# Optimization experiments

Measured on AMD Instinct MI355X. Metric: run time of the kernel, lower is better.

## Reference

```python
import jax, jax.numpy as jnp
import numpy as np

EPS = 1e-5

def _mvn(feat):
    # instance-norm style mean/std over spatial dims; torch .var is unbiased (ddof=1)
    b, c = feat.shape[:2]
    flat = feat.reshape(b, c, -1)
    mu = flat.mean(-1)[:, :, None, None]
    std = jnp.sqrt(flat.var(-1, ddof=1) + EPS)[:, :, None, None]
    return (feat - mu) / std

def setup_inputs() -> dict:
    key = jax.random.key(0)
    ks = jax.random.split(key, 10)
    B, C, H, W = 4, 512, 64, 64
    sc = 0.05
    return {
        "content": jax.random.normal(ks[0], (B, C, H, W), jnp.float32),
        "style": jax.random.normal(ks[1], (B, C, H, W), jnp.float32),
        "content_key": jax.random.normal(ks[2], (B, C, H, W), jnp.float32),
        "style_key": jax.random.normal(ks[3], (B, C, H, W), jnp.float32),
        "Wf": jax.random.normal(ks[4], (C, C), jnp.float32) * sc,
        "bf": jax.random.normal(ks[5], (C,), jnp.float32) * sc,
        "Wg": jax.random.normal(ks[6], (C, C), jnp.float32) * sc,
        "bg": jax.random.normal(ks[7], (C,), jnp.float32) * sc,
        "Wh": jax.random.normal(ks[8], (C, C), jnp.float32) * sc,
        "bh": jax.random.normal(ks[9], (C,), jnp.float32) * sc,
    }

def reference(content, style, content_key, style_key, Wf, bf, Wg, bg, Wh, bh):
    b, C, h, w = content.shape
    hs, ws = style.shape[2], style.shape[3]
    n, m = h * w, hs * ws
    # 1x1 convs are per-pixel linear maps
    Fq = jnp.einsum('oc,bcn->bno', Wf, content_key.reshape(b, -1, n)) + bf      # [b, n, ck]
    G = jnp.einsum('oc,bcn->bon', Wg, style_key.reshape(b, -1, m)) + bg[:, None]  # [b, ck, m]
    V = jnp.einsum('oc,bcn->bno', Wh, style.reshape(b, C, m)) + bh              # [b, m, C]
    S = jax.nn.softmax(jnp.einsum('bnc,bcm->bnm', Fq, G), axis=-1)              # [b, n, m]
    mean = jnp.einsum('bnm,bmc->bnc', S, V)                                     # attention-weighted mean
    m2 = jnp.einsum('bnm,bmc->bnc', S, V * V)                                   # weighted second moment
    std = jnp.sqrt(jax.nn.relu(m2 - mean * mean))
    mean = mean.reshape(b, h, w, C).transpose(0, 3, 1, 2)
    std = std.reshape(b, h, w, C).transpose(0, 3, 1, 2)
    return std * _mvn(content) + mean
```

## Files before the change

### kernel.cpp

```cpp
#include <hip/hip_runtime.h>
#include <math.h>

#define BATCH 4
#define C 512
#define N 4096
#define M 4096
#define MSPLIT 4

typedef __attribute__((ext_vector_type(8))) short short8;
typedef __attribute__((ext_vector_type(8))) __bf16 bf16x8;
typedef __attribute__((ext_vector_type(4))) float f32x4;

static __device__ __forceinline__ unsigned short f2bf(float x) {
    unsigned u = __float_as_uint(x);
    u += 0x7fff + ((u >> 16) & 1);
    return (unsigned short)(u >> 16);
}
static __device__ __forceinline__ float bf2f(unsigned short h) {
    return __uint_as_float(((unsigned)h) << 16);
}
static __device__ __forceinline__ f32x4 mfma_bf16(short8 a, short8 b, f32x4 c) {
    return __builtin_amdgcn_mfma_f32_16x16x32_bf16(
        __builtin_bit_cast(bf16x8, a), __builtin_bit_cast(bf16x8, b), c, 0, 0, 0);
}
static __device__ __forceinline__ void gload16(const void* g, void* l) {
    __builtin_amdgcn_global_load_lds(
        (const __attribute__((address_space(1))) void*)g,
        (__attribute__((address_space(3))) void*)l, 16, 0, 0);
}

__global__ __launch_bounds__(256) void wsplit_kernel(
    const float* __restrict__ W, unsigned short* __restrict__ hi,
    unsigned short* __restrict__ lo)
{
    int i = blockIdx.x * 256 + threadIdx.x;
    float v = W[i];
    unsigned short h = f2bf(v);
    hi[i] = h;
    lo[i] = f2bf(v - bf2f(h));
}

__global__ __launch_bounds__(256) void linear_fg_mfma(
    const float* __restrict__ in,
    const unsigned short* __restrict__ Whi, const unsigned short* __restrict__ Wlo,
    const float* __restrict__ bias,
    unsigned short* __restrict__ out_hi, unsigned short* __restrict__ out_lo)
{
    __shared__ float in_s[32][68];
    __shared__ __align__(16) unsigned short wh_s[64][40];
    __shared__ __align__(16) unsigned short wl_s[64][40];
    const int tid = threadIdx.x;
    const int n0 = blockIdx.x * 64, o0 = blockIdx.y * 64;
    const int w = tid >> 6, lane = tid & 63;
    const int wrow = w >> 1, wcol = w & 1;
    const int lr = lane & 15, q = lane >> 4;
    f32x4 acc[2][2];
    #pragma unroll
    for (int i = 0; i < 2; ++i)
        #pragma unroll
        for (int j = 0; j < 2; ++j) acc[i][j] = (f32x4){0.f, 0.f, 0.f, 0.f};

    for (int kc = 0; kc < C; kc += 32) {
        __syncthreads();
        #pragma unroll
        for (int it = 0; it < 2; ++it) {
            int idx = tid + it * 256;
            int k = idx >> 4, seg = idx & 15;
            *(float4*)&in_s[k][seg * 4] =
                *(const float4*)&in[(size_t)(kc + k) * N + n0 + seg * 4];
        }
        {
            int o = tid >> 2, sg = tid & 3;
            *(float4*)&wh_s[o][sg * 8] = *(const float4*)&Whi[(size_t)(o0 + o) * 512 + kc + sg * 8];
            *(float4*)&wl_s[o][sg * 8] = *(const float4*)&Wlo[(size_t)(o0 + o) * 512 + kc + sg * 8];
        }
        __syncthreads();
        short8 ah[2], al[2], bh[2], bl[2];
        #pragma unroll
        for (int i = 0; i < 2; ++i) {
            int n = wrow * 32 + i * 16 + lr;
            #pragma unroll
            for (int j = 0; j < 8; ++j) {
                float f = in_s[q * 8 + j][n];
                unsigned short h = f2bf(f);
                ah[i][j] = (short)h;
                al[i][j] = (short)f2bf(f - bf2f(h));
            }
        }
        #pragma unroll
        for (int j = 0; j < 2; ++j) {
            int o = wcol * 32 + j * 16 + lr;
            bh[j] = *(const short8*)&wh_s[o][q * 8];
            bl[j] = *(const short8*)&wl_s[o][q * 8];
        }
        #pragma unroll
        for (int i = 0; i < 2; ++i)
            #pragma unroll
            for (int j = 0; j < 2; ++j) {
                acc[i][j] = mfma_bf16(ah[i], bh[j], acc[i][j]);
                acc[i][j] = mfma_bf16(ah[i], bl[j], acc[i][j]);
                acc[i][j] = mfma_bf16(al[i], bh[j], acc[i][j]);
            }
    }
    #pragma unroll
    for (int i = 0; i < 2; ++i)
        #pragma unroll
        for (int j = 0; j < 2; ++j) {
            int o = o0 + wcol * 32 + j * 16 + lr;
            float bo = bias[o];
            #pragma unroll
            for (int r = 0; r < 4; ++r) {
                int n = n0 + wrow * 32 + i * 16 + q * 4 + r;
                float v = acc[i][j][r] + bo;
                unsigned short h = f2bf(v);
                out_hi[(size_t)n * 512 + o] = h;
                out_lo[(size_t)n * 512 + o] = f2bf(v - bf2f(h));
            }
        }
}

__global__ __launch_bounds__(256) void linear_v_mfma(
    const float* __restrict__ in,
    const unsigned short* __restrict__ Whi, const unsigned short* __restrict__ Wlo,
    const float* __restrict__ bias,
    unsigned short* __restrict__ vhT, unsigned short* __restrict__ v2hT,
    unsigned short* __restrict__ v2lT)
{
    __shared__ float in_s[32][68];
    __shared__ __align__(16) unsigned short wh_s[64][40];
    __shared__ __align__(16) unsigned short wl_s[64][40];
    const int tid = threadIdx.x;
    const int m0 = blockIdx.x * 64, o0 = blockIdx.y * 64;
    const int w = tid >> 6, lane = tid & 63;
    const int wrow = w >> 1, wcol = w & 1;
    const int lr = lane & 15, q = lane >> 4;
    f32x4 acc[2][2];
    #pragma unroll
    for (int i = 0; i < 2; ++i)
        #pragma unroll
        for (int j = 0; j < 2; ++j) acc[i][j] = (f32x4){0.f, 0.f, 0.f, 0.f};

    for (int kc = 0; kc < C; kc += 32) {
        __syncthreads();
        #pragma unroll
        for (int it = 0; it < 2; ++it) {
            int idx = tid + it * 256;
            int k = idx >> 4, seg = idx & 15;
            *(float4*)&in_s[k][seg * 4] =
                *(const float4*)&in[(size_t)(kc + k) * N + m0 + seg * 4];
        }
        {
            int o = tid >> 2, sg = tid & 3;
            *(float4*)&wh_s[o][sg * 8] = *(const float4*)&Whi[(size_t)(o0 + o) * 512 + kc + sg * 8];
            *(float4*)&wl_s[o][sg * 8] = *(const float4*)&Wlo[(size_t)(o0 + o) * 512 + kc + sg * 8];
        }
        __syncthreads();
        short8 ah[2], al[2], bh[2], bl[2];
        #pragma unroll
        for (int i = 0; i < 2; ++i) {
            int o = wrow * 32 + i * 16 + lr;
            ah[i] = *(const short8*)&wh_s[o][q * 8];
            al[i] = *(const short8*)&wl_s[o][q * 8];
        }
        #pragma unroll
        for (int j = 0; j < 2; ++j) {
            int m = wcol * 32 + j * 16 + lr;
            #pragma unroll
            for (int t = 0; t < 8; ++t) {
                float f = in_s[q * 8 + t][m];
                unsigned short h = f2bf(f);
                bh[j][t] = (short)h;
                bl[j][t] = (short)f2bf(f - bf2f(h));
            }
        }
        #pragma unroll
        for (int i = 0; i < 2; ++i)
            #pragma unroll
            for (int j = 0; j < 2; ++j) {
                acc[i][j] = mfma_bf16(ah[i], bh[j], acc[i][j]);
                acc[i][j] = mfma_bf16(ah[i], bl[j], acc[i][j]);
                acc[i][j] = mfma_bf16(al[i], bh[j], acc[i][j]);
            }
    }
    #pragma unroll
    for (int i = 0; i < 2; ++i)
        #pragma unroll
        for (int r = 0; r < 4; ++r) {
            int o = o0 + wrow * 32 + i * 16 + q * 4 + r;
            float bo = bias[o];
            const int swz = (o & 3) << 3;
            #pragma unroll
            for (int j = 0; j < 2; ++j) {
                int m = m0 + wcol * 32 + j * 16 + lr;
                float v = acc[i][j][r] + bo;
                unsigned short vh = f2bf(v);
                float vhf = bf2f(vh);
                float vsq = vhf * vhf;
                unsigned short v2h = f2bf(vsq);
                unsigned short v2l = f2bf(vsq - bf2f(v2h));
                size_t off = (size_t)o * M + (m ^ swz);
                vhT[off] = vh;
                v2hT[off] = v2h;
                v2lT[off] = v2l;
            }
        }
}

__global__ __launch_bounds__(256) void logits_mfma_kernel(
    const unsigned short* __restrict__ Ah, const unsigned short* __restrict__ Al,
    const unsigned short* __restrict__ Bh, const unsigned short* __restrict__ Bl,
    float* __restrict__ S)
{
    __shared__ __align__(16) unsigned short Ah_s[128 * 32];
    __shared__ __align__(16) unsigned short Al_s[128 * 32];
    __shared__ __align__(16) unsigned short Bh_s[128 * 32];
    __shared__ __align__(16) unsigned short Bl_s[128 * 32];
    const int tid = threadIdx.x;
    const int n0 = blockIdx.y * 128, m0 = blockIdx.x * 128;
    const int w = tid >> 6, lane = tid & 63;
    const int wrow = w >> 1, wcol = w & 1;
    const int lr = lane & 15, q = lane >> 4;
    const int srow = lane >> 2, scol = (lane & 3) * 8;
    f32x4 acc[4][4];
    #pragma unroll
    for (int i = 0; i < 4; ++i)
        #pragma unroll
        for (int j = 0; j < 4; ++j)
            acc[i][j] = (f32x4){0.f, 0.f, 0.f, 0.f};

    for (int kc = 0; kc < C; kc += 32) {
        __syncthreads();
        #pragma unroll
        for (int g2 = 0; g2 < 2; ++g2) {
            int g = w * 2 + g2;
            size_t ga = (size_t)(n0 + g * 16 + srow) * C + kc + scol;
            size_t gb = (size_t)(m0 + g * 16 + srow) * C + kc + scol;
            int lo = g * 512;
            gload16(&Ah[ga], &Ah_s[lo]);
            gload16(&Al[ga], &Al_s[lo]);
            gload16(&Bh[gb], &Bh_s[lo]);
            gload16(&Bl[gb], &Bl_s[lo]);
        }
        __syncthreads();
        short8 ah[4], al[4], bh[4], bl[4];
        #pragma unroll
        for (int i = 0; i < 4; ++i) {
            int ro = (wrow * 64 + i * 16 + lr) * 32 + q * 8;
            int co = (wcol * 64 + i * 16 + lr) * 32 + q * 8;
            ah[i] = *(const short8*)&Ah_s[ro];
            al[i] = *(const short8*)&Al_s[ro];
            bh[i] = *(const short8*)&Bh_s[co];
            bl[i] = *(const short8*)&Bl_s[co];
        }
        #pragma unroll
        for (int i = 0; i < 4; ++i)
            #pragma unroll
            for (int j = 0; j < 4; ++j) {
                acc[i][j] = mfma_bf16(ah[i], bh[j], acc[i][j]);
                acc[i][j] = mfma_bf16(ah[i], bl[j], acc[i][j]);
                acc[i][j] = mfma_bf16(al[i], bh[j], acc[i][j]);
            }
    }
    #pragma unroll
    for (int i = 0; i < 4; ++i) {
        int nb = n0 + wrow * 64 + i * 16 + q * 4;
        #pragma unroll
        for (int j = 0; j < 4; ++j) {
            int m = m0 + wcol * 64 + j * 16 + lr;
            #pragma unroll
            for (int r = 0; r < 4; ++r)
                S[(size_t)(nb + r) * M + m] = acc[i][j][r];
        }
    }
}

__global__ __launch_bounds__(256) void rowstat_p_kernel(
    const float* __restrict__ S, unsigned short* __restrict__ P,
    float* __restrict__ rsum)
{
    const int n = blockIdx.x;
    const int tid = threadIdx.x;
    const float* row = S + (size_t)n * M;
    float v[16];
    #pragma unroll
    for (int i = 0; i < 16; ++i) v[i] = row[tid + i * 256];
    float lm = -INFINITY;
    #pragma unroll
    for (int i = 0; i < 16; ++i) lm = fmaxf(lm, v[i]);
    #pragma unroll
    for (int off = 32; off > 0; off >>= 1) lm = fmaxf(lm, __shfl_xor(lm, off, 64));
    __shared__ float red[4];
    __shared__ float redsum[4];
    const int wid = tid >> 6, lane = tid & 63;
    if (lane == 0) red[wid] = lm;
    __syncthreads();
    const float rm = fmaxf(fmaxf(red[0], red[1]), fmaxf(red[2], red[3]));
    float ls = 0.f;
    unsigned short* prow = P + (size_t)n * M;
    const int swz = (n & 3) << 3;
    #pragma unroll
    for (int i = 0; i < 16; ++i) {
        float p = __expf(v[i] - rm);
        unsigned short pb = f2bf(p);
        prow[(tid + i * 256) ^ swz] = pb;
        ls += bf2f(pb);
    }
    #pragma unroll
    for (int off = 32; off > 0; off >>= 1) ls += __shfl_xor(ls, off, 64);
    if (lane == 0) redsum[wid] = ls;
    __syncthreads();
    if (tid == 0) rsum[n] = redsum[0] + redsum[1] + redsum[2] + redsum[3];
}

__global__ __launch_bounds__(256) void apply_partial_kernel(
    const unsigned short* __restrict__ P, const unsigned short* __restrict__ VhT,
    const unsigned short* __restrict__ V2hT, const unsigned short* __restrict__ V2lT,
    float* __restrict__ accm_p, float* __restrict__ acc2_p)
{
    __shared__ __align__(16) unsigned short P_s[128 * 32];
    __shared__ __align__(16) unsigned short Vh_s[128 * 32];
    __shared__ __align__(16) unsigned short V2h_s[128 * 32];
    __shared__ __align__(16) unsigned short V2l_s[128 * 32];
    const int tid = threadIdx.x;
    const int c0 = blockIdx.x * 128, n0 = blockIdx.y * 128;
    const int z = blockIdx.z;
    const int w = tid >> 6, lane = tid & 63;
    const int wrow = w >> 1, wcol = w & 1;
    const int lr = lane & 15, q = lane >> 4;
    const int srow = lane >> 2, scol = (lane & 3) * 8;
    f32x4 accm[4][4], acc2[4][4];
    #pragma unroll
    for (int i = 0; i < 4; ++i)
        #pragma unroll
        for (int j = 0; j < 4; ++j) {
            accm[i][j] = (f32x4){0.f, 0.f, 0.f, 0.f};
            acc2[i][j] = (f32x4){0.f, 0.f, 0.f, 0.f};
        }

    const int mbeg = z * (M / MSPLIT);
    for (int mc = mbeg; mc < mbeg + M / MSPLIT; mc += 32) {
        __syncthreads();
        #pragma unroll
        for (int g2 = 0; g2 < 2; ++g2) {
            int g = w * 2 + g2;
            size_t gp = (size_t)(n0 + g * 16 + srow) * M + mc + scol;
            size_t gv = (size_t)(c0 + g * 16 + srow) * M + mc + scol;
            int lo = g * 512;
            gload16(&P[gp],    &P_s[lo]);
            gload16(&VhT[gv],  &Vh_s[lo]);
            gload16(&V2hT[gv], &V2h_s[lo]);
            gload16(&V2lT[gv], &V2l_s[lo]);
        }
        __syncthreads();
        short8 a[4];
        #pragma unroll
        for (int i = 0; i < 4; ++i) {
            int row = wrow * 64 + i * 16 + lr;
            a[i] = *(const short8*)&P_s[row * 32 + (q * 8 ^ ((row & 3) << 3))];
        }
        #pragma unroll
        for (int j = 0; j < 4; ++j) {
            int crow = wcol * 64 + j * 16 + lr;
            int off = crow * 32 + (q * 8 ^ ((crow & 3) << 3));
            short8 bh  = *(const short8*)&Vh_s[off];
            short8 b2h = *(const short8*)&V2h_s[off];
            short8 b2l = *(const short8*)&V2l_s[off];
            #pragma unroll
            for (int i = 0; i < 4; ++i) {
                accm[i][j] = mfma_bf16(a[i], bh,  accm[i][j]);
                acc2[i][j] = mfma_bf16(a[i], b2h, acc2[i][j]);
                acc2[i][j] = mfma_bf16(a[i], b2l, acc2[i][j]);
            }
        }
    }
    const size_t pbase = (size_t)z * N * C;
    #pragma unroll
    for (int i = 0; i < 4; ++i) {
        int nb = n0 + wrow * 64 + i * 16 + q * 4;
        #pragma unroll
        for (int j = 0; j < 4; ++j) {
            int c = c0 + wcol * 64 + j * 16 + lr;
            #pragma unroll
            for (int r = 0; r < 4; ++r) {
                size_t off = pbase + (size_t)(nb + r) * C + c;
                accm_p[off] = accm[i][j][r];
                acc2_p[off] = acc2[i][j][r];
            }
        }
    }
}

__global__ __launch_bounds__(256) void combine_kernel(
    const float* __restrict__ accm_p, const float* __restrict__ acc2_p,
    const float* __restrict__ rsum, float* __restrict__ meanw,
    float* __restrict__ stdw)
{
    const size_t idx = ((size_t)blockIdx.x * 256 + threadIdx.x) * 4;
    const int n = (int)(idx >> 9);
    const float inv = 1.0f / rsum[n];
    float sm[4] = {0.f, 0.f, 0.f, 0.f}, s2[4] = {0.f, 0.f, 0.f, 0.f};
    #pragma unroll
    for (int z = 0; z < MSPLIT; ++z) {
        float4 a = *(const float4*)&accm_p[(size_t)z * N * C + idx];
        float4 b = *(const float4*)&acc2_p[(size_t)z * N * C + idx];
        sm[0] += a.x; sm[1] += a.y; sm[2] += a.z; sm[3] += a.w;
        s2[0] += b.x; s2[1] += b.y; s2[2] += b.z; s2[3] += b.w;
    }
    float4 mnv, sdv;
    float* mp = (float*)&mnv;
    float* sp = (float*)&sdv;
    #pragma unroll
    for (int k = 0; k < 4; ++k) {
        float mn = sm[k] * inv;
        float m2 = s2[k] * inv;
        mp[k] = mn;
        sp[k] = sqrtf(fmaxf(m2 - mn * mn, 0.f));
    }
    *(float4*)&meanw[idx] = mnv;
    *(float4*)&stdw[idx]  = sdv;
}

__global__ __launch_bounds__(256) void mvn_kernel(
    const float* __restrict__ content, float* __restrict__ mu, float* __restrict__ rstd)
{
    const int c = blockIdx.x;
    const int tid = threadIdx.x;
    const float* row = content + (size_t)c * N;
    float s = 0.f, ss = 0.f;
    for (int i = tid; i < N; i += 256) {
        float v = row[i];
        s += v;
        ss = fmaf(v, v, ss);
    }
    #pragma unroll
    for (int off = 32; off > 0; off >>= 1) {
        s  += __shfl_xor(s,  off, 64);
        ss += __shfl_xor(ss, off, 64);
    }
    __shared__ float rs[4], rss[4];
    const int wid = tid >> 6, lane = tid & 63;
    if (lane == 0) { rs[wid] = s; rss[wid] = ss; }
    __syncthreads();
    if (tid == 0) {
        float st = rs[0] + rs[1] + rs[2] + rs[3];
        float sst = rss[0] + rss[1] + rss[2] + rss[3];
        float m = st / (float)N;
        float var = (sst - st * st / (float)N) / (float)(N - 1);
        mu[c] = m;
        rstd[c] = rsqrtf(var + 1e-5f);
    }
}

__global__ __launch_bounds__(256) void final_kernel(
    const float* __restrict__ content, const float* __restrict__ meanw,
    const float* __restrict__ stdw, const float* __restrict__ mu,
    const float* __restrict__ rstd, float* __restrict__ out)
{
    __shared__ float mn_s[32][33], sd_s[32][33];
    const int tid = threadIdx.x;
    const int n0 = blockIdx.x * 32;
    const int c0 = blockIdx.y * 32;
    const int tx = tid & 31, ty = tid >> 5;
    #pragma unroll
    for (int i = 0; i < 4; ++i) {
        int n = ty + i * 8;
        mn_s[tx][n] = meanw[(size_t)(n0 + n) * C + c0 + tx];
        sd_s[tx][n] = stdw [(size_t)(n0 + n) * C + c0 + tx];
    }
    __syncthreads();
    #pragma unroll
    for (int i = 0; i < 4; ++i) {
        int c = ty + i * 8;
        float m = mu[c0 + c], r = rstd[c0 + c];
        size_t off = (size_t)(c0 + c) * N + n0 + tx;
        float x = content[off];
        out[off] = sd_s[c][tx] * (x - m) * r + mn_s[c][tx];
    }
}

extern "C" void kernel_launch(void* const* d_in, const int* in_sizes, int n_in,
                              void* d_out, int out_size, void* d_ws, size_t ws_size,
                              hipStream_t stream)
{
    const float* content = (const float*)d_in[0];
    const float* style   = (const float*)d_in[1];
    const float* ckey    = (const float*)d_in[2];
    const float* skey    = (const float*)d_in[3];
    const float* Wf      = (const float*)d_in[4];
    const float* bf      = (const float*)d_in[5];
    const float* Wg      = (const float*)d_in[6];
    const float* bg      = (const float*)d_in[7];
    const float* Wh      = (const float*)d_in[8];
    const float* bh      = (const float*)d_in[9];
    float* out = (float*)d_out;

    const size_t sz_w  = (size_t)512 * 512 * 2;
    const size_t sz_S  = (size_t)N * M * 4;
    const size_t sz_FG = (size_t)N * C * 2;
    const size_t sz_P  = (size_t)N * M * 2;
    const size_t sz_V  = (size_t)C * M * 2;

    char* p = (char*)d_ws;
    auto alloc = [&](size_t bytes) {
        char* r = p;
        p += (bytes + 255) & ~(size_t)255;
        return r;
    };
    unsigned short* WfH = (unsigned short*)alloc(sz_w);
    unsigned short* WfL = (unsigned short*)alloc(sz_w);
    unsigned short* WgH = (unsigned short*)alloc(sz_w);
    unsigned short* WgL = (unsigned short*)alloc(sz_w);
    unsigned short* WhH = (unsigned short*)alloc(sz_w);
    unsigned short* WhL = (unsigned short*)alloc(sz_w);
    float* S = (float*)alloc(sz_S);
    unsigned short* Fh = (unsigned short*)alloc(sz_FG);
    unsigned short* Fl = (unsigned short*)alloc(sz_FG);
    unsigned short* Gh = (unsigned short*)alloc(sz_FG);
    unsigned short* Gl = (unsigned short*)alloc(sz_FG);
    unsigned short* P    = (unsigned short*)alloc(sz_P);
    unsigned short* VhT  = (unsigned short*)alloc(sz_V);
    unsigned short* V2hT = (unsigned short*)alloc(sz_V);
    unsigned short* V2lT = (unsigned short*)alloc(sz_V);
    float* rsum  = (float*)alloc((size_t)N * 4);
    float* meanw = (float*)alloc((size_t)N * C * 4);
    float* stdw  = (float*)alloc((size_t)N * C * 4);
    float* mu    = (float*)alloc((size_t)C * 4);
    float* rstd  = (float*)alloc((size_t)C * 4);

    float* accm_p = S;
    float* acc2_p = S + (size_t)MSPLIT * N * C;

    wsplit_kernel<<<dim3(1024), 256, 0, stream>>>(Wf, WfH, WfL);
    wsplit_kernel<<<dim3(1024), 256, 0, stream>>>(Wg, WgH, WgL);
    wsplit_kernel<<<dim3(1024), 256, 0, stream>>>(Wh, WhH, WhL);

    for (int b = 0; b < BATCH; ++b) {
        const size_t fo = (size_t)b * C * N;
        linear_fg_mfma<<<dim3(N / 64, C / 64), 256, 0, stream>>>(ckey + fo, WfH, WfL, bf, Fh, Fl);
        linear_fg_mfma<<<dim3(M / 64, C / 64), 256, 0, stream>>>(skey + fo, WgH, WgL, bg, Gh, Gl);
        linear_v_mfma<<<dim3(M / 64, C / 64), 256, 0, stream>>>(style + fo, WhH, WhL, bh,
                                                                VhT, V2hT, V2lT);
        logits_mfma_kernel<<<dim3(M / 128, N / 128), 256, 0, stream>>>(Fh, Fl, Gh, Gl, S);
        rowstat_p_kernel<<<dim3(N), 256, 0, stream>>>(S, P, rsum);
        apply_partial_kernel<<<dim3(C / 128, N / 128, MSPLIT), 256, 0, stream>>>(
            P, VhT, V2hT, V2lT, accm_p, acc2_p);
        combine_kernel<<<dim3(N * C / 1024), 256, 0, stream>>>(
            accm_p, acc2_p, rsum, meanw, stdw);
        mvn_kernel<<<dim3(C), 256, 0, stream>>>(content + fo, mu, rstd);
        final_kernel<<<dim3(N / 32, C / 32), 256, 0, stream>>>(
            content + fo, meanw, stdw, mu, rstd, out + fo);
    }
}
```

Measured before the change: 1.211 ms.

## Double-buffer apply_partial LDS tiles and halve channel tile width

The apply_partial kernel now double-buffers its LDS tiles, issuing the global loads for the next 32-wide M chunk before computing on the current one, which removes one barrier per iteration. The channel tile shrinks from 128 to 64, halving accumulator registers and doubling the grid to raise occupancy. The cost is that each P tile is now loaded from global memory twice as often, since twice as many blocks cover the channel dimension.

```diff
diff --git a/kernel.cpp b/kernel.cpp
--- a/kernel.cpp
+++ b/kernel.cpp
@@ -317,69 +317,77 @@
     const unsigned short* __restrict__ V2hT, const unsigned short* __restrict__ V2lT,
     float* __restrict__ accm_p, float* __restrict__ acc2_p)
 {
-    __shared__ __align__(16) unsigned short P_s[128 * 32];
-    __shared__ __align__(16) unsigned short Vh_s[128 * 32];
-    __shared__ __align__(16) unsigned short V2h_s[128 * 32];
-    __shared__ __align__(16) unsigned short V2l_s[128 * 32];
-    const int tid = threadIdx.x;
-    const int c0 = blockIdx.x * 128, n0 = blockIdx.y * 128;
+    __shared__ __align__(16) unsigned short P_s[2][128 * 32];
+    __shared__ __align__(16) unsigned short Vh_s[2][64 * 32];
+    __shared__ __align__(16) unsigned short V2h_s[2][64 * 32];
+    __shared__ __align__(16) unsigned short V2l_s[2][64 * 32];
+    const int tid = threadIdx.x;
+    const int c0 = blockIdx.x * 64, n0 = blockIdx.y * 128;
     const int z = blockIdx.z;
     const int w = tid >> 6, lane = tid & 63;
     const int wrow = w >> 1, wcol = w & 1;
     const int lr = lane & 15, q = lane >> 4;
     const int srow = lane >> 2, scol = (lane & 3) * 8;
-    f32x4 accm[4][4], acc2[4][4];
+    f32x4 accm[4][2], acc2[4][2];
     #pragma unroll
     for (int i = 0; i < 4; ++i)
         #pragma unroll
-        for (int j = 0; j < 4; ++j) {
+        for (int j = 0; j < 2; ++j) {
             accm[i][j] = (f32x4){0.f, 0.f, 0.f, 0.f};
             acc2[i][j] = (f32x4){0.f, 0.f, 0.f, 0.f};
         }
 
     const int mbeg = z * (M / MSPLIT);
-    for (int mc = mbeg; mc < mbeg + M / MSPLIT; mc += 32) {
-        __syncthreads();
+    const size_t vrow = (size_t)(c0 + w * 16 + srow) * M + scol;
+
+    auto STAGE = [&](int buf, int mc) {
         #pragma unroll
         for (int g2 = 0; g2 < 2; ++g2) {
             int g = w * 2 + g2;
-            size_t gp = (size_t)(n0 + g * 16 + srow) * M + mc + scol;
-            size_t gv = (size_t)(c0 + g * 16 + srow) * M + mc + scol;
-            int lo = g * 512;
-            gload16(&P[gp],    &P_s[lo]);
-            gload16(&VhT[gv],  &Vh_s[lo]);
-            gload16(&V2hT[gv], &V2h_s[lo]);
-            gload16(&V2lT[gv], &V2l_s[lo]);
-        }
-        __syncthreads();
-        short8 a[4];
+            gload16(&P[(size_t)(n0 + g * 16 + srow) * M + mc + scol], &P_s[buf][g * 512]);
+        }
+        gload16(&VhT [vrow + mc], &Vh_s[buf][w * 512]);
+        gload16(&V2hT[vrow + mc], &V2h_s[buf][w * 512]);
+        gload16(&V2lT[vrow + mc], &V2l_s[buf][w * 512]);
+    };
+
+    const int NT = (M / MSPLIT) / 32;
+    STAGE(0, mbeg);
+    int cur = 0;
+    for (int t = 0; t < NT; ++t) {
+        __syncthreads();
+        if (t + 1 < NT) STAGE(cur ^ 1, mbeg + (t + 1) * 32);
+        short8 a[4], bh[2], b2h[2], b2l[2];
         #pragma unroll
         for (int i = 0; i < 4; ++i) {
             int row = wrow * 64 + i * 16 + lr;
-            a[i] = *(const short8*)&P_s[row * 32 + (q * 8 ^ ((row & 3) << 3))];
-        }
-        #pragma unroll
-        for (int j = 0; j < 4; ++j) {
-            int crow = wcol * 64 + j * 16 + lr;
+            a[i] = *(const short8*)&P_s[cur][row * 32 + (q * 8 ^ ((row & 3) << 3))];
+        }
+        #pragma unroll
+        for (int j = 0; j < 2; ++j) {
+            int crow = wcol * 32 + j * 16 + lr;
             int off = crow * 32 + (q * 8 ^ ((crow & 3) << 3));
-            short8 bh  = *(const short8*)&Vh_s[off];
-            short8 b2h = *(const short8*)&V2h_s[off];
-            short8 b2l = *(const short8*)&V2l_s[off];
-            #pragma unroll
-            for (int i = 0; i < 4; ++i) {
-                accm[i][j] = mfma_bf16(a[i], bh,  accm[i][j]);
-                acc2[i][j] = mfma_bf16(a[i], b2h, acc2[i][j]);
-                acc2[i][j] = mfma_bf16(a[i], b2l, acc2[i][j]);
-            }
-        }
+            bh[j]  = *(const short8*)&Vh_s[cur][off];
+            b2h[j] = *(const short8*)&V2h_s[cur][off];
+            b2l[j] = *(const short8*)&V2l_s[cur][off];
+        }
+        #pragma unroll
+        for (int i = 0; i < 4; ++i)
+            #pragma unroll
+            for (int j = 0; j < 2; ++j) {
+                accm[i][j] = mfma_bf16(a[i], bh[j],  accm[i][j]);
+                acc2[i][j] = mfma_bf16(a[i], b2h[j], acc2[i][j]);
+                acc2[i][j] = mfma_bf16(a[i], b2l[j], acc2[i][j]);
+            }
+        cur ^= 1;
     }
     const size_t pbase = (size_t)z * N * C;
     #pragma unroll
     for (int i = 0; i < 4; ++i) {
         int nb = n0 + wrow * 64 + i * 16 + q * 4;
         #pragma unroll
-        for (int j = 0; j < 4; ++j) {
-            int c = c0 + wcol * 64 + j * 16 + lr;
+        for (int j = 0; j < 2; ++j) {
+            int c = c0 + wcol * 32 + j * 16 + lr;
             #pragma unroll
             for (int r = 0; r < 4; ++r) {
                 size_t off = pbase + (size_t)(nb + r) * C + c;
@@ -542,7 +550,7 @@
                                                                 VhT, V2hT, V2lT);
         logits_mfma_kernel<<<dim3(M / 128, N / 128), 256, 0, stream>>>(Fh, Fl, Gh, Gl, S);
         rowstat_p_kernel<<<dim3(N), 256, 0, stream>>>(S, P, rsum);
-        apply_partial_kernel<<<dim3(C / 128, N / 128, MSPLIT), 256, 0, stream>>>(
+        apply_partial_kernel<<<dim3(C / 64, N / 128, MSPLIT), 256, 0, stream>>>(
             P, VhT, V2hT, V2lT, accm_p, acc2_p);
         combine_kernel<<<dim3(N * C / 1024), 256, 0, stream>>>(
             accm_p, acc2_p, rsum, meanw, stdw);
```

New measurement: 1.195 ms. No clear change (-1.4%).
